# Optimization experiments

Measured on AMD Instinct MI355X. Metric: run time of the kernel, lower is better.

## Reference

```python
import jax, jax.numpy as jnp
import numpy as np

INPUT_SIZE = 256
HIDDEN = 512
OUTPUT = 128
NUM_LAYERS = 2
BATCH = 20  # hard-coded by init_hidden(20) in the original module
SEQ = 2048


def _uniform(key, shape, bound):
    return jax.random.uniform(key, shape, jnp.float32, -bound, bound)


def setup_inputs() -> dict:
    key = jax.random.key(0)
    ks = jax.random.split(key, 12)
    k = 1.0 / np.sqrt(HIDDEN)  # torch nn.RNN init: U(-1/sqrt(H), 1/sqrt(H))
    inp = {
        "x": jax.random.normal(ks[0], (BATCH, SEQ, INPUT_SIZE), jnp.float32),
        "h0": jnp.zeros((NUM_LAYERS, BATCH, HIDDEN), jnp.float32),
        "W_ih0": _uniform(ks[1], (HIDDEN, INPUT_SIZE), k),
        "W_hh0": _uniform(ks[2], (HIDDEN, HIDDEN), k),
        "b_ih0": _uniform(ks[3], (HIDDEN,), k),
        "b_hh0": _uniform(ks[4], (HIDDEN,), k),
        "W_ih1": _uniform(ks[5], (HIDDEN, HIDDEN), k),
        "W_hh1": _uniform(ks[6], (HIDDEN, HIDDEN), k),
        "b_ih1": _uniform(ks[7], (HIDDEN,), k),
        "b_hh1": _uniform(ks[8], (HIDDEN,), k),
        "W_fc": _uniform(ks[9], (OUTPUT, HIDDEN), 1.0 / np.sqrt(HIDDEN)),
        "b_fc": _uniform(ks[10], (OUTPUT,), 1.0 / np.sqrt(HIDDEN)),
    }
    return inp


def _rnn_layer(inp, h_init, W_ih, W_hh, b_ih, b_hh):
    # Precompute input projection for all timesteps: [B, T, H]
    pre = jnp.einsum('bti,hi->bth', inp, W_ih) + b_ih

    def step(h, p_t):
        h_new = jnp.tanh(p_t + h @ W_hh.T + b_hh)  # [B, H]
        return h_new, h_new

    _, hs = jax.lax.scan(step, h_init, jnp.swapaxes(pre, 0, 1))  # hs: [T, B, H]
    return jnp.swapaxes(hs, 0, 1)  # [B, T, H]


def reference(x, h0, W_ih0, W_hh0, b_ih0, b_hh0, W_ih1, W_hh1, b_ih1, b_hh1, W_fc, b_fc):
    # 2-layer tanh RNN (eval mode: inter-layer dropout inactive) + final Linear on last timestep
    out = _rnn_layer(x, h0[0], W_ih0, W_hh0, b_ih0, b_hh0)
    out = _rnn_layer(out, h0[1], W_ih1, W_hh1, b_ih1, b_hh1)
    return out[:, -1, :] @ W_fc.T + b_fc  # [B, OUTPUT]
```

## Files before the change

kernel.cpp:

```cpp
#include <hip/hip_runtime.h>

#define TSEQ 2048
#define NB   20
#define NIN  256
#define NH   512
#define NOUT 128

typedef unsigned int   u32;
typedef unsigned short u16;
typedef _Float16 f16x2 __attribute__((ext_vector_type(2)));

#define SM_W     0
#define SM_HX    131072
#define SM_INP   (131072 + 2048)
#define SMEM_BYTES (131072 + 2048 + 2048)

__device__ __forceinline__ u32 packh2(float a, float b) {
  f16x2 p; p.x = (_Float16)a; p.y = (_Float16)b;
  return __builtin_bit_cast(u32, p);
}

__device__ __forceinline__ float dot2(u32 w, u32 h, float acc) {
  return __builtin_amdgcn_fdot2(__builtin_bit_cast(f16x2, w),
                                __builtin_bit_cast(f16x2, h), acc, false);
}

__device__ __forceinline__ int acq(const int* p) {
  return __hip_atomic_load(p, __ATOMIC_ACQUIRE, __HIP_MEMORY_SCOPE_AGENT);
}
__device__ __forceinline__ void rel(int* p, int v) {
  __hip_atomic_store(p, v, __ATOMIC_RELEASE, __HIP_MEMORY_SCOPE_AGENT);
}

__device__ __forceinline__ void lds_barrier() {
  asm volatile("s_waitcnt lgkmcnt(0)\n\ts_barrier" ::: "memory");
}

template<int CTRL>
__device__ __forceinline__ float dpp_add(float x) {
  int v = __builtin_amdgcn_update_dpp(0, __builtin_bit_cast(int, x), CTRL, 0xF, 0xF, true);
  return x + __builtin_bit_cast(float, v);
}

template<int CTRL>
__device__ __forceinline__ u32 dpp_mov_u32(u32 x) {
  return (u32)__builtin_amdgcn_update_dpp(0, (int)x, CTRL, 0xF, 0xF, true);
}

__device__ __forceinline__ float bfly_sum16(float a) {
  a = dpp_add<0xB1>(a);
  a = dpp_add<0x4E>(a);
  a = dpp_add<0x124>(a);
  a = dpp_add<0x128>(a);
  return a;
}

__device__ __forceinline__ float fast_tanh(float x) {
  float xc = fminf(fmaxf(x, -15.f), 15.f);
  float e = __builtin_amdgcn_exp2f(xc * 2.8853900817779268f);
  return (e - 1.f) * __builtin_amdgcn_rcpf(e + 1.f);
}

__device__ __forceinline__ int hx_gran_off(int g, int c) {
  int pg = (g ^ (g >> 2)) & 15;
  return 64 * pg + 16 * (c ^ (g & 3));
}

__global__ __launch_bounds__(512, 2) void rnn_persist(
    const float* __restrict__ x,    const float* __restrict__ h0,
    const float* __restrict__ Wih0, const float* __restrict__ Whh0,
    const float* __restrict__ bih0, const float* __restrict__ bhh0,
    const float* __restrict__ Wih1, const float* __restrict__ Whh1,
    const float* __restrict__ bih1, const float* __restrict__ bhh1,
    u16* __restrict__ pre0, u32* __restrict__ out0,
    u16* __restrict__ pre1, float* __restrict__ h1f,
    int* __restrict__ flags)
{
  extern __shared__ char smem[];
  const int tid = threadIdx.x;
  const int bid = blockIdx.x;

  if (bid < 40) {
    u32* inp = (u32*)(smem + SM_INP);
    const int b = bid >> 1, half = bid & 1, t0 = half * 1024;
    const int n = tid;
    u32 wr[128];
    const float4* W4 = (const float4*)(Wih0 + (size_t)n * NIN);
#pragma unroll
    for (int j = 0; j < 64; j++) {
      float4 w = W4[j];
      wr[2*j] = packh2(w.x, w.y); wr[2*j+1] = packh2(w.z, w.w);
    }
    const float bias = bih0[n];
    const float* xb = x + ((size_t)b * TSEQ + t0) * NIN;
    u16* op = pre0 + ((size_t)b * TSEQ + t0) * NH;

    float2 r = make_float2(0.f, 0.f);
    if (tid < 128) r = ((const float2*)xb)[tid];
    int cur = 0;
    for (int t = 0; t < 1024; t++) {
      if (tid < 128) inp[cur * 256 + tid] = packh2(r.x, r.y);
      __syncthreads();
      if (t + 1 < 1024 && tid < 128)
        r = ((const float2*)(xb + (size_t)(t + 1) * NIN))[tid];
      float a0 = bias, a1 = 0.f;
      const uint4* xp = (const uint4*)(inp + cur * 256);
#pragma unroll
      for (int j = 0; j < 32; j++) {
        uint4 hv = xp[j];
        a0 = dot2(wr[4*j+0], hv.x, a0); a1 = dot2(wr[4*j+1], hv.y, a1);
        a0 = dot2(wr[4*j+2], hv.z, a0); a1 = dot2(wr[4*j+3], hv.w, a1);
      }
      op[((size_t)(t >> 3) * NH + n) * 8 + (t & 7)] =
          __builtin_bit_cast(u16, (_Float16)(a0 + a1));
      cur ^= 1;
      if (((t + 1) & 7) == 0) {
        __syncthreads();
        if (tid == 0) rel(flags + bid * 32, t + 1);
      }
    }
    return;
  }

  if (bid >= 60 && bid < 140) {
    uint2* WL  = (uint2*)(smem + SM_W);
    u32*   inp = (u32*)(smem + SM_INP);
    const int b = (bid - 60) >> 2, sub = (bid - 60) & 3;
    const int n = tid;
    u32 wr[192];
    const float4* W4 = (const float4*)(Wih1 + (size_t)n * NH);
#pragma unroll
    for (int j = 0; j < 96; j++) {
      float4 w = W4[j];
      wr[2*j] = packh2(w.x, w.y); wr[2*j+1] = packh2(w.z, w.w);
    }
#pragma unroll
    for (int j2 = 0; j2 < 32; j2++) {
      float4 w = W4[96 + j2];
      WL[j2 * NH + n] = make_uint2(packh2(w.x, w.y), packh2(w.z, w.w));
    }
    const float bias = bih1[n];
    __syncthreads();

    const u32* ip = out0 + (size_t)b * TSEQ * 256;
    u16* op = pre1 + (size_t)b * TSEQ * NH;
    const int* flagOut0 = flags + (40 + b) * 32;
    int* flagMy = flags + (60 + b * 4 + sub) * 32;
    int seen = 0, cur = 0;
#pragma unroll 1
    for (int c = sub; c < TSEQ / 8; c += 4) {
      const int tbase = c * 8;
      while (seen < tbase + 8) seen = acq(flagOut0);
      u32 rin = (tid < 256) ? ip[(size_t)tbase * 256 + tid] : 0;
#pragma unroll 1
      for (int qq = 0; qq < 8; qq++) {
        const int t = tbase + qq;
        if (tid < 256) inp[cur * 256 + tid] = rin;
        __syncthreads();
        if (qq + 1 < 8 && tid < 256) rin = ip[(size_t)(t + 1) * 256 + tid];
        float a0 = bias, a1 = 0.f;
        const uint4* hp4 = (const uint4*)(inp + cur * 256);
#pragma unroll
        for (int j = 0; j < 48; j++) {
          uint4 hv = hp4[j];
          a0 = dot2(wr[4*j+0], hv.x, a0); a1 = dot2(wr[4*j+1], hv.y, a1);
          a0 = dot2(wr[4*j+2], hv.z, a0); a1 = dot2(wr[4*j+3], hv.w, a1);
        }
#pragma unroll
        for (int jj = 0; jj < 16; jj++) {
          uint4 hv = hp4[48 + jj];
          uint2 w0 = WL[(2*jj)   * NH + n];
          uint2 w1 = WL[(2*jj+1) * NH + n];
          a0 = dot2(w0.x, hv.x, a0); a1 = dot2(w0.y, hv.y, a1);
          a0 = dot2(w1.x, hv.z, a0); a1 = dot2(w1.y, hv.w, a1);
        }
        op[((size_t)(t >> 3) * NH + n) * 8 + (t & 7)] =
            __builtin_bit_cast(u16, (_Float16)(a0 + a1));
        cur ^= 1;
      }
      __syncthreads();
      if (tid == 0) rel(flagMy, tbase + 8);
    }
    return;
  }

  const bool isL0 = (bid < 60);
  const int b = isL0 ? (bid - 40) : (bid - 140);
  const float* Wg = isL0 ? Whh0 : Whh1;
  const float* bp = isL0 ? bhh0 : bhh1;

  uint4* WLw4 = (uint4*)(smem + SM_W);
  char*  hxc  = smem + SM_HX;

  const int lam = tid & 15;
  const int ns  = tid >> 4;

  u32 wj[12][16];
#pragma unroll
  for (int j = 0; j < 12; j++) {
    const float4* Wr = (const float4*)(Wg + (size_t)(16 * ns + j) * NH + 32 * lam);
#pragma unroll
    for (int k4 = 0; k4 < 8; k4++) {
      float4 w = Wr[k4];
      wj[j][2*k4] = packh2(w.x, w.y); wj[j][2*k4+1] = packh2(w.z, w.w);
    }
  }
#pragma unroll
  for (int j = 12; j < 16; j++) {
    const float4* Wr = (const float4*)(Wg + (size_t)(16 * ns + j) * NH + 32 * lam);
#pragma unroll
    for (int q = 0; q < 4; q++) {
      float4 wA = Wr[2*q], wB = Wr[2*q+1];
      WLw4[((j - 12) * 4 + q) * 512 + tid] =
          make_uint4(packh2(wA.x, wA.y), packh2(wA.z, wA.w),
                     packh2(wB.x, wB.y), packh2(wB.z, wB.w));
    }
  }
  const float bias = bp[tid];

  int hadr[4];
#pragma unroll
  for (int c = 0; c < 4; c++) hadr[c] = hx_gran_off(lam, c);
  const int wg = (tid >> 5) & 15, wc = (tid >> 3) & 3;
  const int waddr = hx_gran_off(wg, wc) + (tid & 7) * 2;

  *(u16*)(hxc + waddr) =
      __builtin_bit_cast(u16, (_Float16)h0[((isL0 ? 0 : 1) * NB + b) * NH + tid]);
  __syncthreads();

  const uint4* pin4 =
      (const uint4*)((isL0 ? pre0 : pre1) + (size_t)b * TSEQ * NH);
  u32* o0p = out0 + (size_t)b * TSEQ * 256;
  int* flagOut0 = flags + (40 + b) * 32;
  const int* f0 = flags + (b * 2 + 0) * 32;
  const int* f1 = flags + (b * 2 + 1) * 32;
  const int* fpA = flags + (60 + b * 4 + 0) * 32;
  const int* fpB = flags + (60 + b * 4 + 1) * 32;
  const int* fpC = flags + (60 + b * 4 + 2) * 32;
  const int* fpD = flags + (60 + b * 4 + 3) * 32;
  int s0 = 0, s1 = 0, sA = 0, sB = 0, sC = 0, sD = 0;

  if (isL0) { while (s0 < 8)  s0 = acq(f0); }
  else      { while (sA < 8)  sA = acq(fpA); }
  uint4 pcur4 = pin4[tid];
  if (isL0) { while (s0 < 16) s0 = acq(f0); }
  else      { while (sB < 16) sB = acq(fpB); }
  uint4 pnext4 = pin4[512 + tid];

  float hlast = 0.f;
#pragma unroll 1
  for (int c = 0; c < TSEQ / 8; c++) {
#pragma unroll 1
    for (int q = 0; q < 8; q++) {
      const int t = c * 8 + q;
      const int rbase = (t & 1) << 10;
      const int wbase = rbase ^ 1024;

      const uint4 hv0 = *(const uint4*)(hxc + rbase + hadr[0]);
      const uint4 hv1 = *(const uint4*)(hxc + rbase + hadr[1]);
      const uint4 hv2 = *(const uint4*)(hxc + rbase + hadr[2]);
      const uint4 hv3 = *(const uint4*)(hxc + rbase + hadr[3]);

      float red = 0.f;
#pragma unroll
      for (int j = 0; j < 12; j++) {
        float a = 0.f;
        a = dot2(wj[j][0],  hv0.x, a); a = dot2(wj[j][1],  hv0.y, a);
        a = dot2(wj[j][2],  hv0.z, a); a = dot2(wj[j][3],  hv0.w, a);
        a = dot2(wj[j][4],  hv1.x, a); a = dot2(wj[j][5],  hv1.y, a);
        a = dot2(wj[j][6],  hv1.z, a); a = dot2(wj[j][7],  hv1.w, a);
        a = dot2(wj[j][8],  hv2.x, a); a = dot2(wj[j][9],  hv2.y, a);
        a = dot2(wj[j][10], hv2.z, a); a = dot2(wj[j][11], hv2.w, a);
        a = dot2(wj[j][12], hv3.x, a); a = dot2(wj[j][13], hv3.y, a);
        a = dot2(wj[j][14], hv3.z, a); a = dot2(wj[j][15], hv3.w, a);
        a = bfly_sum16(a);
        red = (lam == j) ? a : red;
      }
#pragma unroll
      for (int j = 0; j < 4; j++) {
        const uint4 wv0 = WLw4[(j * 4 + 0) * 512 + tid];
        const uint4 wv1 = WLw4[(j * 4 + 1) * 512 + tid];
        const uint4 wv2 = WLw4[(j * 4 + 2) * 512 + tid];
        const uint4 wv3 = WLw4[(j * 4 + 3) * 512 + tid];
        float a = 0.f;
        a = dot2(wv0.x, hv0.x, a); a = dot2(wv0.y, hv0.y, a);
        a = dot2(wv0.z, hv0.z, a); a = dot2(wv0.w, hv0.w, a);
        a = dot2(wv1.x, hv1.x, a); a = dot2(wv1.y, hv1.y, a);
        a = dot2(wv1.z, hv1.z, a); a = dot2(wv1.w, hv1.w, a);
        a = dot2(wv2.x, hv2.x, a); a = dot2(wv2.y, hv2.y, a);
        a = dot2(wv2.z, hv2.z, a); a = dot2(wv2.w, hv2.w, a);
        a = dot2(wv3.x, hv3.x, a); a = dot2(wv3.y, hv3.y, a);
        a = dot2(wv3.z, hv3.z, a); a = dot2(wv3.w, hv3.w, a);
        a = bfly_sum16(a);
        red = (lam == 12 + j) ? a : red;
      }

      const u32 wlo  = (q & 4) ? pcur4.z : pcur4.x;
      const u32 whi  = (q & 4) ? pcur4.w : pcur4.y;
      const u32 wsel = (q & 2) ? whi : wlo;
      const u16 pq   = (u16)((q & 1) ? (wsel >> 16) : (wsel & 0xffffu));

      const float h = fast_tanh(red + bias + (float)__builtin_bit_cast(_Float16, pq));
      hlast = h;
      const u16 h16 = __builtin_bit_cast(u16, (_Float16)h);
      *(u16*)(hxc + wbase + waddr) = h16;

      if (isL0) {
        u32 v = (u32)h16;
        u32 nb = dpp_mov_u32<0xB1>(v);
        if (!(tid & 1)) o0p[(size_t)t * 256 + (tid >> 1)] = v | (nb << 16);
      }

      if (q == 7) __syncthreads();
      else        lds_barrier();
    }

    if (isL0 && tid == 0) rel(flagOut0, c * 8 + 8);

    pcur4 = pnext4;
    if (c < TSEQ / 8 - 2) {
      const int c2 = c + 2;
      const int need = 8 * (c2 + 1);
      if (isL0) {
        if (c2 < 128) { while (s0 < need)        s0 = acq(f0); }
        else          { while (s1 < need - 1024) s1 = acq(f1); }
      } else {
        const int w = c2 & 3;
        if      (w == 0) { while (sA < need) sA = acq(fpA); }
        else if (w == 1) { while (sB < need) sB = acq(fpB); }
        else if (w == 2) { while (sC < need) sC = acq(fpC); }
        else             { while (sD < need) sD = acq(fpD); }
      }
      pnext4 = pin4[(size_t)c2 * 512 + tid];
    }
  }

  if (!isL0) h1f[(size_t)b * NH + tid] = hlast;
}

__global__ void fc_kernel(const float* __restrict__ h1f, const float* __restrict__ Wfc,
                          const float* __restrict__ bfc, float* __restrict__ out) {
  const int b = blockIdx.x, o = threadIdx.x;
  __shared__ float hs[NH];
  for (int i = o; i < NH; i += NOUT) hs[i] = h1f[(size_t)b * NH + i];
  __syncthreads();
  const float4* w4 = (const float4*)(Wfc + (size_t)o * NH);
  const float4* h4 = (const float4*)hs;
  float acc = bfc[o];
#pragma unroll 8
  for (int j = 0; j < NH / 4; j++) {
    float4 w = w4[j], h = h4[j];
    acc += w.x * h.x + w.y * h.y + w.z * h.z + w.w * h.w;
  }
  out[(size_t)b * NOUT + o] = acc;
}

extern "C" void kernel_launch(void* const* d_in, const int* in_sizes, int n_in,
                              void* d_out, int out_size, void* d_ws, size_t ws_size,
                              hipStream_t stream) {
  const float* x    = (const float*)d_in[0];
  const float* h0   = (const float*)d_in[1];
  const float* Wih0 = (const float*)d_in[2];
  const float* Whh0 = (const float*)d_in[3];
  const float* bih0 = (const float*)d_in[4];
  const float* bhh0 = (const float*)d_in[5];
  const float* Wih1 = (const float*)d_in[6];
  const float* Whh1 = (const float*)d_in[7];
  const float* bih1 = (const float*)d_in[8];
  const float* bhh1 = (const float*)d_in[9];
  const float* Wfc  = (const float*)d_in[10];
  const float* bfc  = (const float*)d_in[11];
  float* out = (float*)d_out;

  char* ws = (char*)d_ws;
  size_t off = 0;
  u16* pre0 = (u16*)(ws + off); off += (size_t)NB * TSEQ * NH * 2;
  u32* out0 = (u32*)(ws + off); off += (size_t)NB * TSEQ * (NH / 2) * 4;
  u16* pre1 = (u16*)(ws + off); off += (size_t)NB * TSEQ * NH * 2;
  float* h1f = (float*)(ws + off); off += (size_t)NB * NH * 4;
  int* flags = (int*)(ws + off);
  const size_t flagbytes = 160 * 32 * sizeof(int);

  hipMemsetAsync(flags, 0, flagbytes, stream);
  hipFuncSetAttribute((const void*)rnn_persist,
                      hipFuncAttributeMaxDynamicSharedMemorySize, SMEM_BYTES);
  rnn_persist<<<160, 512, SMEM_BYTES, stream>>>(
      x, h0, Wih0, Whh0, bih0, bhh0, Wih1, Whh1, bih1, bhh1,
      pre0, out0, pre1, h1f, flags);
  fc_kernel<<<NB, NOUT, 0, stream>>>(h1f, Wfc, bfc, out);
}
```

Before: 4.236 ms.

## Replace per-row butterfly reductions with transposed DPP reduction tree and sleepy spins

The recurrent matvec previously ran a full 4-stage DPP butterfly on each of 16 rows and then picked one lane's result. It now reassigns weight rows so that each group of four rows forms a reduction-transpose tree: partial sums are merged with select-and-add across DPP stages. This cuts the DPP and select count per timestep from 64 adds to roughly 28. Spin-wait loops on flags now insert s_sleep between polls, which reduces memory traffic contention but may add wake-up latency on the critical path.

```diff
diff --git a/kernel.cpp b/kernel.cpp
--- a/kernel.cpp
+++ b/kernel.cpp
@@ -31,6 +31,12 @@
 __device__ __forceinline__ void rel(int* p, int v) {
   __hip_atomic_store(p, v, __ATOMIC_RELEASE, __HIP_MEMORY_SCOPE_AGENT);
 }
+__device__ __forceinline__ void spin_until(const int* p, int need, int& seen) {
+  while (seen < need) {
+    seen = acq(p);
+    if (seen < need) __builtin_amdgcn_s_sleep(1);
+  }
+}
 
 __device__ __forceinline__ void lds_barrier() {
   asm volatile("s_waitcnt lgkmcnt(0)\n\ts_barrier" ::: "memory");
@@ -45,14 +51,6 @@
 template<int CTRL>
 __device__ __forceinline__ u32 dpp_mov_u32(u32 x) {
   return (u32)__builtin_amdgcn_update_dpp(0, (int)x, CTRL, 0xF, 0xF, true);
-}
-
-__device__ __forceinline__ float bfly_sum16(float a) {
-  a = dpp_add<0xB1>(a);
-  a = dpp_add<0x4E>(a);
-  a = dpp_add<0x124>(a);
-  a = dpp_add<0x128>(a);
-  return a;
 }
 
 __device__ __forceinline__ float fast_tanh(float x) {
@@ -150,7 +148,7 @@
 #pragma unroll 1
     for (int c = sub; c < TSEQ / 8; c += 4) {
       const int tbase = c * 8;
-      while (seen < tbase + 8) seen = acq(flagOut0);
+      spin_until(flagOut0, tbase + 8, seen);
       u32 rin = (tid < 256) ? ip[(size_t)tbase * 256 + tid] : 0;
 #pragma unroll 1
       for (int qq = 0; qq < 8; qq++) {
@@ -197,21 +195,24 @@
 
   u32 wj[12][16];
 #pragma unroll
-  for (int j = 0; j < 12; j++) {
-    const float4* Wr = (const float4*)(Wg + (size_t)(16 * ns + j) * NH + 32 * lam);
-#pragma unroll
-    for (int k4 = 0; k4 < 8; k4++) {
-      float4 w = Wr[k4];
-      wj[j][2*k4] = packh2(w.x, w.y); wj[j][2*k4+1] = packh2(w.z, w.w);
-    }
-  }
-#pragma unroll
-  for (int j = 12; j < 16; j++) {
-    const float4* Wr = (const float4*)(Wg + (size_t)(16 * ns + j) * NH + 32 * lam);
+  for (int g = 0; g < 4; g++) {
+#pragma unroll
+    for (int m = 0; m < 3; m++) {
+      const float4* Wr = (const float4*)(Wg + (size_t)(16 * ns + 4 * g + m) * NH + 32 * lam);
+#pragma unroll
+      for (int k4 = 0; k4 < 8; k4++) {
+        float4 w = Wr[k4];
+        wj[3*g+m][2*k4] = packh2(w.x, w.y); wj[3*g+m][2*k4+1] = packh2(w.z, w.w);
+      }
+    }
+  }
+#pragma unroll
+  for (int g = 0; g < 4; g++) {
+    const float4* Wr = (const float4*)(Wg + (size_t)(16 * ns + 4 * g + 3) * NH + 32 * lam);
 #pragma unroll
     for (int q = 0; q < 4; q++) {
       float4 wA = Wr[2*q], wB = Wr[2*q+1];
-      WLw4[((j - 12) * 4 + q) * 512 + tid] =
+      WLw4[(4 * g + q) * 512 + tid] =
           make_uint4(packh2(wA.x, wA.y), packh2(wA.z, wA.w),
                      packh2(wB.x, wB.y), packh2(wB.z, wB.w));
     }
@@ -223,6 +224,7 @@
   for (int c = 0; c < 4; c++) hadr[c] = hx_gran_off(lam, c);
   const int wg = (tid >> 5) & 15, wc = (tid >> 3) & 3;
   const int waddr = hx_gran_off(wg, wc) + (tid & 7) * 2;
+  const bool b0 = (tid & 1), b1 = (tid & 2), b2 = (tid & 4), b3 = (tid & 8);
 
   *(u16*)(hxc + waddr) =
       __builtin_bit_cast(u16, (_Float16)h0[((isL0 ? 0 : 1) * NB + b) * NH + tid]);
@@ -240,12 +242,45 @@
   const int* fpD = flags + (60 + b * 4 + 3) * 32;
   int s0 = 0, s1 = 0, sA = 0, sB = 0, sC = 0, sD = 0;
 
-  if (isL0) { while (s0 < 8)  s0 = acq(f0); }
-  else      { while (sA < 8)  sA = acq(fpA); }
+  if (isL0) { spin_until(f0, 8, s0); }  else { spin_until(fpA, 8, sA); }
   uint4 pcur4 = pin4[tid];
-  if (isL0) { while (s0 < 16) s0 = acq(f0); }
-  else      { while (sB < 16) sB = acq(fpB); }
+  if (isL0) { spin_until(f0, 16, s0); } else { spin_until(fpB, 16, sB); }
   uint4 pnext4 = pin4[512 + tid];
+
+#define ROW16(acc, WR)                                              \
+    acc = dot2(WR[0],  hv0.x, acc); acc = dot2(WR[1],  hv0.y, acc); \
+    acc = dot2(WR[2],  hv0.z, acc); acc = dot2(WR[3],  hv0.w, acc); \
+    acc = dot2(WR[4],  hv1.x, acc); acc = dot2(WR[5],  hv1.y, acc); \
+    acc = dot2(WR[6],  hv1.z, acc); acc = dot2(WR[7],  hv1.w, acc); \
+    acc = dot2(WR[8],  hv2.x, acc); acc = dot2(WR[9],  hv2.y, acc); \
+    acc = dot2(WR[10], hv2.z, acc); acc = dot2(WR[11], hv2.w, acc); \
+    acc = dot2(WR[12], hv3.x, acc); acc = dot2(WR[13], hv3.y, acc); \
+    acc = dot2(WR[14], hv3.z, acc); acc = dot2(WR[15], hv3.w, acc)
+
+#define GROUP(gi, OUT)                                               \
+  {                                                                  \
+    const uint4 wvA = WLw4[(4*gi + 0) * 512 + tid];                  \
+    const uint4 wvB = WLw4[(4*gi + 1) * 512 + tid];                  \
+    float a0 = 0.f, a1 = 0.f, a2 = 0.f, a3 = 0.f;                    \
+    ROW16(a0, wj[3*gi+0]);                                           \
+    a3 = dot2(wvA.x, hv0.x, a3); a3 = dot2(wvA.y, hv0.y, a3);        \
+    a3 = dot2(wvA.z, hv0.z, a3); a3 = dot2(wvA.w, hv0.w, a3);        \
+    const uint4 wvC = WLw4[(4*gi + 2) * 512 + tid];                  \
+    const uint4 wvD = WLw4[(4*gi + 3) * 512 + tid];                  \
+    ROW16(a1, wj[3*gi+1]);                                           \
+    a3 = dot2(wvB.x, hv1.x, a3); a3 = dot2(wvB.y, hv1.y, a3);        \
+    a3 = dot2(wvB.z, hv1.z, a3); a3 = dot2(wvB.w, hv1.w, a3);        \
+    ROW16(a2, wj[3*gi+2]);                                           \
+    a3 = dot2(wvC.x, hv2.x, a3); a3 = dot2(wvC.y, hv2.y, a3);        \
+    a3 = dot2(wvC.z, hv2.z, a3); a3 = dot2(wvC.w, hv2.w, a3);        \
+    a3 = dot2(wvD.x, hv3.x, a3); a3 = dot2(wvD.y, hv3.y, a3);        \
+    a3 = dot2(wvD.z, hv3.z, a3); a3 = dot2(wvD.w, hv3.w, a3);        \
+    float t0 = dpp_add<0xB1>(a0), t1 = dpp_add<0xB1>(a1);            \
+    float t2 = dpp_add<0xB1>(a2), t3 = dpp_add<0xB1>(a3);            \
+    float u0 = b0 ? t1 : t0, u1 = b0 ? t3 : t2;                      \
+    u0 = dpp_add<0x4E>(u0); u1 = dpp_add<0x4E>(u1);                  \
+    OUT = b1 ? u1 : u0;                                              \
+  }
 
   float hlast = 0.f;
 #pragma unroll 1
@@ -261,39 +296,13 @@
       const uint4 hv2 = *(const uint4*)(hxc + rbase + hadr[2]);
       const uint4 hv3 = *(const uint4*)(hxc + rbase + hadr[3]);
 
-      float red = 0.f;
-#pragma unroll
-      for (int j = 0; j < 12; j++) {
-        float a = 0.f;
-        a = dot2(wj[j][0],  hv0.x, a); a = dot2(wj[j][1],  hv0.y, a);
-        a = dot2(wj[j][2],  hv0.z, a); a = dot2(wj[j][3],  hv0.w, a);
-        a = dot2(wj[j][4],  hv1.x, a); a = dot2(wj[j][5],  hv1.y, a);
-        a = dot2(wj[j][6],  hv1.z, a); a = dot2(wj[j][7],  hv1.w, a);
-        a = dot2(wj[j][8],  hv2.x, a); a = dot2(wj[j][9],  hv2.y, a);
-        a = dot2(wj[j][10], hv2.z, a); a = dot2(wj[j][11], hv2.w, a);
-        a = dot2(wj[j][12], hv3.x, a); a = dot2(wj[j][13], hv3.y, a);
-        a = dot2(wj[j][14], hv3.z, a); a = dot2(wj[j][15], hv3.w, a);
-        a = bfly_sum16(a);
-        red = (lam == j) ? a : red;
-      }
-#pragma unroll
-      for (int j = 0; j < 4; j++) {
-        const uint4 wv0 = WLw4[(j * 4 + 0) * 512 + tid];
-        const uint4 wv1 = WLw4[(j * 4 + 1) * 512 + tid];
-        const uint4 wv2 = WLw4[(j * 4 + 2) * 512 + tid];
-        const uint4 wv3 = WLw4[(j * 4 + 3) * 512 + tid];
-        float a = 0.f;
-        a = dot2(wv0.x, hv0.x, a); a = dot2(wv0.y, hv0.y, a);
-        a = dot2(wv0.z, hv0.z, a); a = dot2(wv0.w, hv0.w, a);
-        a = dot2(wv1.x, hv1.x, a); a = dot2(wv1.y, hv1.y, a);
-        a = dot2(wv1.z, hv1.z, a); a = dot2(wv1.w, hv1.w, a);
-        a = dot2(wv2.x, hv2.x, a); a = dot2(wv2.y, hv2.y, a);
-        a = dot2(wv2.z, hv2.z, a); a = dot2(wv2.w, hv2.w, a);
-        a = dot2(wv3.x, hv3.x, a); a = dot2(wv3.y, hv3.y, a);
-        a = dot2(wv3.z, hv3.z, a); a = dot2(wv3.w, hv3.w, a);
-        a = bfly_sum16(a);
-        red = (lam == 12 + j) ? a : red;
-      }
+      float G0, G1, G2, G3;
+      GROUP(0, G0); GROUP(1, G1); GROUP(2, G2); GROUP(3, G3);
+      G0 = dpp_add<0x124>(G0); G1 = dpp_add<0x124>(G1);
+      G2 = dpp_add<0x124>(G2); G3 = dpp_add<0x124>(G3);
+      float r0 = b2 ? G1 : G0, r1 = b2 ? G3 : G2;
+      r0 = dpp_add<0x128>(r0); r1 = dpp_add<0x128>(r1);
+      const float red = b3 ? r1 : r0;
 
       const u32 wlo  = (q & 4) ? pcur4.z : pcur4.x;
       const u32 whi  = (q & 4) ? pcur4.w : pcur4.y;
@@ -322,18 +331,20 @@
       const int c2 = c + 2;
       const int need = 8 * (c2 + 1);
       if (isL0) {
-        if (c2 < 128) { while (s0 < need)        s0 = acq(f0); }
-        else          { while (s1 < need - 1024) s1 = acq(f1); }
+        if (c2 < 128) { spin_until(f0, need, s0); }
+        else          { spin_until(f1, need - 1024, s1); }
       } else {
         const int w = c2 & 3;
-        if      (w == 0) { while (sA < need) sA = acq(fpA); }
-        else if (w == 1) { while (sB < need) sB = acq(fpB); }
-        else if (w == 2) { while (sC < need) sC = acq(fpC); }
-        else             { while (sD < need) sD = acq(fpD); }
+        if      (w == 0) { spin_until(fpA, need, sA); }
+        else if (w == 1) { spin_until(fpB, need, sB); }
+        else if (w == 2) { spin_until(fpC, need, sC); }
+        else             { spin_until(fpD, need, sD); }
       }
       pnext4 = pin4[(size_t)c2 * 512 + tid];
     }
   }
+#undef GROUP
+#undef ROW16
 
   if (!isL0) h1f[(size_t)b * NH + tid] = hlast;
 }
```

Result: faster. 3.636 ms (-14.2%).
